# Kernel optimization log

Hardware: AMD Instinct MI355X
Metric: run time of the kernel (lower is better)

Reference implementation:

```python
import jax, jax.numpy as jnp
import numpy as np


def lrelu(x):
    return jnp.where(x > 0, x, 0.1 * x)


def setup_inputs() -> dict:
    key = jax.random.key(0)
    ks = jax.random.split(key, 16)
    L, B, E = 160, 16, 512
    C, H, DM, DO = 256, 512, 128, 512  # conv channels, enc_hid, d_mlp, dec_hid

    def rn(k, shape, scale=0.05):
        return jax.random.normal(k, shape, dtype=jnp.float32) * scale

    return {
        "x": rn(ks[0], (L, B, E), 1.0),
        "h": rn(ks[1], (B, H), 1.0),
        "conv_w": rn(ks[2], (C, E, 3)),
        "conv_b": rn(ks[3], (C,)),
        "bn_g": jnp.ones((C,), jnp.float32),
        "bn_b": jnp.zeros((C,), jnp.float32),
        "W1": rn(ks[4], (DM, 2 * (C + 2) + H)),
        "b1": rn(ks[5], (DM,)),
        "W2": rn(ks[6], (DM, DM)), "b2": rn(ks[7], (DM,)),
        "W3": rn(ks[8], (DM, DM)), "b3": rn(ks[9], (DM,)),
        "W4": rn(ks[10], (DM, DM)), "b4": rn(ks[11], (DM,)),
        "W5": rn(ks[12], (DM, DM)), "b5": rn(ks[13], (DM,)),
        "W6": rn(ks[14], (DO, DM)), "b6": rn(ks[15], (DO,)),
    }


def reference(x, h, conv_w, conv_b, bn_g, bn_b,
              W1, b1, W2, b2, W3, b3, W4, b4, W5, b5, W6, b6):
    L, B, E = x.shape
    # --- ConvLayer: Conv1d(k=3, pad=1) -> LeakyReLU(0.1) -> BatchNorm1d (training stats)
    xc = jnp.transpose(x, (1, 2, 0))  # (B, E, L)
    y = jax.lax.conv_general_dilated(xc, conv_w, (1,), [(1, 1)],
                                     dimension_numbers=("NCH", "OIH", "NCH"))
    y = lrelu(y + conv_b[None, :, None])
    mu = y.mean(axis=(0, 2), keepdims=True)
    var = y.var(axis=(0, 2), keepdims=True)  # biased variance (torch training BN)
    y = (y - mu) * jax.lax.rsqrt(var + 1e-5)
    y = y * bn_g[None, :, None] + bn_b[None, :, None]
    y = jnp.transpose(y, (0, 2, 1))  # (B, L, C)

    # --- coordinate features: [(i/sqrt(L)-2)/2, (i % sqrt(L) - 2)/2]
    sL = np.sqrt(L)
    i = jnp.arange(L, dtype=jnp.float32)
    coords = jnp.stack([(i / sL - 2.0) / 2.0, (jnp.mod(i, sL) - 2.0) / 2.0], axis=-1)  # (L, 2)
    xf = jnp.concatenate([y, jnp.broadcast_to(coords[None], (B, L, 2))], axis=-1)  # (B, L, C+2)
    Cp = xf.shape[-1]

    # --- g_mlp first Linear decomposed over [x_i | x_j | h] feature blocks:
    # x_i[b,a,c] = xf[b,c] (varies with dim2); x_j[b,a,c] = cat(xf[b,a], h[b]) (varies with dim1)
    W1i = W1[:, :Cp]            # acts on x_i
    W1jx = W1[:, Cp:2 * Cp]     # acts on x part of x_j
    W1jh = W1[:, 2 * Cp:]       # acts on h part of x_j
    u = jnp.einsum('blc,dc->bld', xf, W1i)                     # (B, L, DM), index = dim2
    v = jnp.einsum('blc,dc->bld', xf, W1jx) + (h @ W1jh.T)[:, None, :]  # (B, L, DM), index = dim1
    z = lrelu(v[:, :, None, :] + u[:, None, :, :] + b1)        # (B, L, L, DM)
    z = lrelu(z @ W2.T + b2)
    z = lrelu(z @ W3.T + b3)
    z = lrelu(z @ W4.T + b4)
    s = z.sum(axis=(1, 2))  # sum over all L*L pairs -> (B, DM)

    # --- f_mlp
    s = lrelu(s @ W5.T + b5)
    return lrelu(s @ W6.T + b6)  # (B, dec_hid)
```

## Files before the change

### kernel.cpp

```cpp
#include <hip/hip_runtime.h>
#include <cstdint>

typedef unsigned short u16;
typedef uint32_t u32;

typedef __bf16 bf16x8 __attribute__((ext_vector_type(8)));
typedef float  f32x2  __attribute__((ext_vector_type(2)));
typedef float  f32x4  __attribute__((ext_vector_type(4)));
typedef float  f32x16 __attribute__((ext_vector_type(16)));
typedef u16    u16x4  __attribute__((ext_vector_type(4)));
typedef u16    u16x8  __attribute__((ext_vector_type(8)));

__device__ __forceinline__ u16 f2bf(float f) {
    u32 x = __float_as_uint(f);
    return (u16)((x + 0x7FFFu + ((x >> 16) & 1u)) >> 16);
}
__device__ __forceinline__ float lrelu(float x) { return fmaxf(x, 0.1f * x); }

__device__ __forceinline__ u32 pack_rn(float lo, float hi) {
    u32 a = __float_as_uint(lo) + 0x8000u;
    u32 b = __float_as_uint(hi) + 0x8000u;
    return __builtin_amdgcn_perm(b, a, 0x07060302u);
}

__global__ __launch_bounds__(256) void k_prep(
    const float* __restrict__ x, const float* __restrict__ conv_w,
    const float* __restrict__ W2, const float* __restrict__ W3, const float* __restrict__ W4,
    const float* __restrict__ b2, const float* __restrict__ b3, const float* __restrict__ b4,
    const float* __restrict__ h, const float* __restrict__ W1,
    u16* __restrict__ xb, u16* __restrict__ wcb_f, u16* __restrict__ wfrag,
    float* __restrict__ W1T4, float* __restrict__ hW, float* __restrict__ zero0)
{
    int blk = blockIdx.x, tid = threadIdx.x;
    if (blk < 1280) {
        int o = (blk * 256 + tid) * 4;
        int e = o & 511;
        int bl = o >> 9;
        int b = bl / 160, l = bl % 160;
        f32x4 v = *(const f32x4*)(x + ((size_t)(l * 16 + b)) * 512 + e);
        u16x4 ov;
        ov[0] = f2bf(v[0]); ov[1] = f2bf(v[1]); ov[2] = f2bf(v[2]); ov[3] = f2bf(v[3]);
        *(u16x4*)&xb[o] = ov;
    } else if (blk < 1472) {
        int g = (blk - 1280) * 256 + tid;
        int lane = g & 63;
        int ks = (g >> 6) % 48;
        int cb = g / 3072;
        int c = cb * 16 + (lane & 15);
        int quad = lane >> 4;
        int k0 = ks * 32 + quad * 8;
        int tap = k0 >> 9, e0 = k0 & 511;
        u16x8 ov;
        #pragma unroll
        for (int j = 0; j < 8; j++)
            ov[j] = f2bf(conv_w[((size_t)c * 512 + e0 + j) * 3 + tap]);
        *(u16x8*)&wcb_f[(size_t)g * 8] = ov;
    } else if (blk < 1526) {
        int o = ((blk - 1472) * 256 + tid) * 4;
        int layer = o / 18432, rem = o % 18432;
        int ks9 = rem >> 11;
        int rem2 = rem & 2047;
        int hh = rem2 >> 10;
        int rem3 = rem2 & 1023;
        int n = rem3 >> 3, j0 = rem3 & 7;
        const float* W = (layer == 0) ? W2 : (layer == 1) ? W3 : W4;
        const float* bi = (layer == 0) ? b2 : (layer == 1) ? b3 : b4;
        u16x4 ov;
        if (ks9 < 8) {
            f32x4 v = *(const f32x4*)(W + (size_t)n * 128 + 16 * ks9 + 8 * hh + j0);
            ov[0] = f2bf(v[0]); ov[1] = f2bf(v[1]); ov[2] = f2bf(v[2]); ov[3] = f2bf(v[3]);
        } else {
            ov[0] = (hh == 0 && j0 == 0) ? f2bf(bi[n]) : (u16)0;
            ov[1] = 0; ov[2] = 0; ov[3] = 0;
        }
        *(u16x4*)&wfrag[o] = ov;
    } else if (blk < 1591) {
        int cq = blk - 1526;
        int t = tid;
        const float* src = (t < 128)
            ? (W1 + (size_t)t * 1028 + cq * 4)
            : (W1 + (size_t)(t - 128) * 1028 + 258 + cq * 4);
        f32x2 v0 = *(const f32x2*)src;
        f32x2 v1 = *(const f32x2*)(src + 2);
        f32x4 v;
        v[0] = v0[0]; v[1] = v0[1];
        v[2] = (cq == 64) ? 0.f : v1[0];
        v[3] = (cq == 64) ? 0.f : v1[1];
        *(f32x4*)&W1T4[((size_t)cq * 256 + t) * 4] = v;
    } else if (blk < 1719) {
        int gid = (blk - 1591) * 256 + tid;
        int outp = gid >> 4, q = gid & 15;
        int b = outp >> 7, d = outp & 127;
        const float* hr = h + (size_t)b * 512;
        const float* wr = W1 + (size_t)d * 1028 + 516;
        float acc = 0.f;
        #pragma unroll
        for (int c = 0; c < 8; c++) {
            int k = c * 64 + q * 4;
            f32x4 hv = *(const f32x4*)(hr + k);
            f32x4 wv = *(const f32x4*)(wr + k);
            acc += hv[0]*wv[0] + hv[1]*wv[1] + hv[2]*wv[2] + hv[3]*wv[3];
        }
        acc += __shfl_xor(acc, 1); acc += __shfl_xor(acc, 2);
        acc += __shfl_xor(acc, 4); acc += __shfl_xor(acc, 8);
        if (q == 0) hW[outp] = acc;
    } else {
        int idx = (blk - 1719) * 256 + tid;
        if (idx < 640) {
            f32x4 z = {0.f, 0.f, 0.f, 0.f};
            *(f32x4*)&zero0[idx * 4] = z;
        }
    }
}

__global__ __launch_bounds__(256, 4) void k_conv(
    const u16* __restrict__ xb, const u16* __restrict__ wcb_f,
    const float* __restrict__ conv_b,
    float* __restrict__ ws_y, float* __restrict__ stats)
{
    __shared__ u16 xs[18 * 520];
    int tid = threadIdx.x, wg = blockIdx.x;
    int rowtile = wg >> 2, cg = wg & 3;
    int b = rowtile / 10, l0 = (rowtile % 10) * 16;

    for (int t = tid; t < 18 * 64; t += 256) {
        int s = t >> 6, ch = t & 63;
        int lg = l0 + s - 1;
        u16x8 v = {};
        if (lg >= 0 && lg < 160)
            v = *(const u16x8*)(xb + ((size_t)(b * 160 + lg)) * 512 + ch * 8);
        *(u16x8*)&xs[s * 520 + ch * 8] = v;
    }
    __syncthreads();

    int lane = tid & 63, w = tid >> 6;
    int row16 = lane & 15, quad = lane >> 4;
    int cb = cg * 4 + w;
    int c_n = cb * 16 + row16;
    const u16* wb = wcb_f + (size_t)cb * 24576;

    f32x4 acc0 = {0,0,0,0};
    for (int ks4 = 0; ks4 < 48; ks4 += 4) {
        bf16x8 wf[4];
        #pragma unroll
        for (int q = 0; q < 4; q++)
            wf[q] = *(const bf16x8*)(wb + (size_t)((ks4 + q) * 64 + lane) * 8);
        #pragma unroll
        for (int q = 0; q < 4; q++) {
            int k = (ks4 + q) * 32 + quad * 8;
            int tap = k >> 9, e = k & 511;
            bf16x8 a0 = *(const bf16x8*)&xs[(row16 + tap) * 520 + e];
            acc0 = __builtin_amdgcn_mfma_f32_16x16x32_bf16(a0, wf[q], acc0, 0, 0, 0);
        }
    }

    float bias = conv_b[c_n];
    float sum = 0.f, sq = 0.f;
    #pragma unroll
    for (int r = 0; r < 4; r++) {
        float v = lrelu(acc0[r] + bias);
        int lr = l0 + quad * 4 + r;
        ws_y[((size_t)(b * 160 + lr)) * 256 + c_n] = v;
        sum += v; sq += v * v;
    }
    sum += __shfl_xor(sum, 16); sum += __shfl_xor(sum, 32);
    sq  += __shfl_xor(sq, 16);  sq  += __shfl_xor(sq, 32);
    if (quad == 0) {
        atomicAdd(&stats[c_n], sum);
        atomicAdd(&stats[256 + c_n], sq);
    }
}

__global__ __launch_bounds__(256) void k_uv(
    const float* __restrict__ ws_y, const float* __restrict__ stats,
    const float* __restrict__ bn_g, const float* __restrict__ bn_b,
    const float* __restrict__ W1T4, const float* __restrict__ b1,
    const float* __restrict__ hW,
    float* __restrict__ uu, float* __restrict__ vv)
{
    __shared__ float a_s[256], c_s[256];
    __shared__ float xfs[4 * 260];
    int tid = threadIdx.x;
    int row0 = blockIdx.x * 4;
    int b = row0 / 160, l0 = row0 % 160;
    {
        int c = tid;
        float mu  = stats[c] * (1.0f / 2560.0f);
        float var = stats[256 + c] * (1.0f / 2560.0f) - mu * mu;
        float rs  = rsqrtf(var + 1e-5f) * bn_g[c];
        a_s[c] = rs;
        c_s[c] = bn_b[c] - mu * rs;
    }
    __syncthreads();
    float sLf = sqrtf(160.0f);
    for (int idx = tid; idx < 4 * 260; idx += 256) {
        int r = idx / 260, c = idx - r * 260;
        int l = l0 + r;
        float v = 0.f;
        if (c < 256) {
            v = ws_y[((size_t)(b * 160 + l)) * 256 + c] * a_s[c] + c_s[c];
        } else if (c == 256) {
            v = ((float)l / sLf - 2.0f) * 0.5f;
        } else if (c == 257) {
            float fi = (float)l;
            float m = fi - floorf(fi / sLf) * sLf;
            v = (m - 2.0f) * 0.5f;
        }
        xfs[r * 260 + c] = v;
    }
    __syncthreads();

    float acc[4] = {0,0,0,0};
    #pragma unroll 4
    for (int cq = 0; cq < 65; cq++) {
        f32x4 w4 = *(const f32x4*)&W1T4[((size_t)cq * 256 + tid) * 4];
        #pragma unroll
        for (int r = 0; r < 4; r++) {
            f32x4 xv = *(const f32x4*)&xfs[r * 260 + cq * 4];
            acc[r] += w4[0]*xv[0] + w4[1]*xv[1] + w4[2]*xv[2] + w4[3]*xv[3];
        }
    }

    bool isv = tid >= 128;
    int d = tid & 127;
    float vadd = isv ? (hW[b * 128 + d] + b1[d]) : 0.f;
    float* dst = isv ? vv : uu;
    #pragma unroll
    for (int r = 0; r < 4; r++)
        dst[((size_t)(b * 160 + l0 + r)) * 128 + d] = acc[r] + vadd;
}

__global__ __launch_bounds__(256, 4) void k_mlp(
    const float* __restrict__ vv, const float* __restrict__ uu,
    const u16* __restrict__ wfrag,
    float* __restrict__ s_glob)
{
    __shared__ __align__(16) u16 Wlds[18432];
    __shared__ float spart[128];
    int tid = threadIdx.x;
    int wave = tid >> 6, lane = tid & 63;
    int h = lane >> 5, lo = lane & 31;
    int b = blockIdx.x / 200, sub = blockIdx.x % 200;
    int tileb = sub * 4 + wave;

    if (tid < 128) spart[tid] = 0.f;

    u32 selv = h ? 0x07060302u : 0x05040100u;
    uint4 biasfrag;
    biasfrag.x = (h == 0) ? 0x00003F80u : 0u;
    biasfrag.y = 0u; biasfrag.z = 0u; biasfrag.w = 0u;

    uint4 B[8];
    f32x16 acc[4];
    float ssum[4];

    int i  = (tileb / 10) * 2  + (lo >> 4);
    int jj = (tileb % 10) * 16 + (lo & 15);
    const float* vr = vv + ((size_t)(b * 160 + i))  * 128 + 8 * h;
    const float* ur = uu + ((size_t)(b * 160 + jj)) * 128 + 8 * h;

    for (int layer = 0; layer < 3; layer++) {
        __syncthreads();
        {
            const uint4* src = (const uint4*)(wfrag + layer * 18432);
            #pragma unroll
            for (int it = 0; it < 9; it++) {
                int idx = it * 256 + tid;
                *(uint4*)&Wlds[idx * 8] = src[idx];
            }
        }
        __syncthreads();

        if (layer == 0) {
            #pragma unroll
            for (int ks = 0; ks < 8; ks++) {
                f32x4 v0 = *(const f32x4*)(vr + 16 * ks);
                f32x4 v1 = *(const f32x4*)(vr + 16 * ks + 4);
                f32x4 u0 = *(const f32x4*)(ur + 16 * ks);
                f32x4 u1 = *(const f32x4*)(ur + 16 * ks + 4);
                uint4 d;
                d.x = pack_rn(lrelu(v0[0]+u0[0]), lrelu(v0[1]+u0[1]));
                d.y = pack_rn(lrelu(v0[2]+u0[2]), lrelu(v0[3]+u0[3]));
                d.z = pack_rn(lrelu(v1[0]+u1[0]), lrelu(v1[1]+u1[1]));
                d.w = pack_rn(lrelu(v1[2]+u1[2]), lrelu(v1[3]+u1[3]));
                B[ks] = d;
            }
        }

        #pragma unroll
        for (int nt = 0; nt < 4; nt++)
            #pragma unroll
            for (int r = 0; r < 16; r++) acc[nt][r] = 0.f;

        #pragma unroll
        for (int ks = 0; ks < 9; ks++) {
            uint4 zu = (ks < 8) ? B[ks] : biasfrag;
            bf16x8 zf = *(bf16x8*)&zu;
            #pragma unroll
            for (int nt = 0; nt < 4; nt++) {
                bf16x8 wf = *(const bf16x8*)&Wlds[(size_t)(ks * 256 + h * 128 + nt * 32 + lo) * 8];
                if (layer < 2)
                    acc[nt] = __builtin_amdgcn_mfma_f32_32x32x16_bf16(wf, zf, acc[nt], 0, 0, 0);
                else
                    acc[nt] = __builtin_amdgcn_mfma_f32_32x32x16_bf16(zf, wf, acc[nt], 0, 0, 0);
            }
        }

        if (layer < 2) {
            #pragma unroll
            for (int nt = 0; nt < 4; nt++) {
                u32 own[4][2], oth[4][2];
                #pragma unroll
                for (int c = 0; c < 4; c++)
                    #pragma unroll
                    for (int p = 0; p < 2; p++)
                        own[c][p] = pack_rn(lrelu(acc[nt][c + 8*p]),
                                            lrelu(acc[nt][c + 4 + 8*p]));
                #pragma unroll
                for (int c = 0; c < 4; c++)
                    #pragma unroll
                    for (int p = 0; p < 2; p++)
                        oth[c][p] = (u32)__shfl_xor((int)own[c][p], 32);
                #pragma unroll
                for (int p = 0; p < 2; p++) {
                    u32 dA0 = __builtin_amdgcn_perm(own[1][p], own[0][p], selv);
                    u32 dB0 = __builtin_amdgcn_perm(oth[1][p], oth[0][p], selv);
                    u32 dA1 = __builtin_amdgcn_perm(own[3][p], own[2][p], selv);
                    u32 dB1 = __builtin_amdgcn_perm(oth[3][p], oth[2][p], selv);
                    uint4 d;
                    d.x = h ? dB0 : dA0;
                    d.y = h ? dB1 : dA1;
                    d.z = h ? dA0 : dB0;
                    d.w = h ? dA1 : dB1;
                    B[2 * nt + p] = d;
                }
            }
        } else {
            #pragma unroll
            for (int nt = 0; nt < 4; nt++) {
                float t = 0.f;
                #pragma unroll
                for (int r = 0; r < 16; r++)
                    t += lrelu(acc[nt][r]);
                ssum[nt] = t;
            }
        }
    }

    #pragma unroll
    for (int nt = 0; nt < 4; nt++) {
        float v = ssum[nt] + __shfl_xor(ssum[nt], 32);
        if (h == 0) atomicAdd(&spart[nt * 32 + lo], v);
    }
    __syncthreads();
    if (tid < 128) atomicAdd(&s_glob[b * 128 + tid], spart[tid]);
}

__global__ __launch_bounds__(256) void k_final(
    const float* __restrict__ s_glob,
    const float* __restrict__ W5, const float* __restrict__ b5,
    const float* __restrict__ W6, const float* __restrict__ b6,
    float* __restrict__ out)
{
    __shared__ float sh[128], t5[128];
    int b = blockIdx.x, tid = threadIdx.x;
    if (tid < 128) sh[tid] = s_glob[b * 128 + tid];
    __syncthreads();
    if (tid < 128) {
        const float* wr = W5 + (size_t)tid * 128;
        float acc = b5[tid];
        #pragma unroll
        for (int k = 0; k < 128; k += 4) {
            f32x4 wv = *(const f32x4*)(wr + k);
            f32x4 sv = *(const f32x4*)&sh[k];
            acc += wv[0]*sv[0] + wv[1]*sv[1] + wv[2]*sv[2] + wv[3]*sv[3];
        }
        t5[tid] = lrelu(acc);
    }
    __syncthreads();
    #pragma unroll
    for (int q = 0; q < 2; q++) {
        int o = q * 256 + tid;
        const float* wr = W6 + (size_t)o * 128;
        float acc = b6[o];
        #pragma unroll
        for (int k = 0; k < 128; k += 4) {
            f32x4 wv = *(const f32x4*)(wr + k);
            f32x4 tv = *(const f32x4*)&t5[k];
            acc += wv[0]*tv[0] + wv[1]*tv[1] + wv[2]*tv[2] + wv[3]*tv[3];
        }
        out[b * 512 + o] = lrelu(acc);
    }
}

extern "C" void kernel_launch(void* const* d_in, const int* in_sizes, int n_in,
                              void* d_out, int out_size, void* d_ws, size_t ws_size,
                              hipStream_t stream)
{
    const float* x      = (const float*)d_in[0];
    const float* h      = (const float*)d_in[1];
    const float* conv_w = (const float*)d_in[2];
    const float* conv_b = (const float*)d_in[3];
    const float* bn_g   = (const float*)d_in[4];
    const float* bn_b   = (const float*)d_in[5];
    const float* W1     = (const float*)d_in[6];
    const float* b1     = (const float*)d_in[7];
    const float* W2     = (const float*)d_in[8];
    const float* b2     = (const float*)d_in[9];
    const float* W3     = (const float*)d_in[10];
    const float* b3     = (const float*)d_in[11];
    const float* W4     = (const float*)d_in[12];
    const float* b4     = (const float*)d_in[13];
    const float* W5     = (const float*)d_in[14];
    const float* b5     = (const float*)d_in[15];
    const float* W6     = (const float*)d_in[16];
    const float* b6     = (const float*)d_in[17];

    char* ws = (char*)d_ws;
    float* s_glob = (float*)(ws + 0);
    float* stats  = (float*)(ws + 8192);
    float* hW     = (float*)(ws + 10240);
    float* ws_y   = (float*)(ws + 18432);
    float* vv     = (float*)(ws + 2639872);
    float* uu     = (float*)(ws + 3950592);
    u16*   xb     = (u16*)  (ws + 5261312);
    u16*   wcb_f  = (u16*)  (ws + 7882752);
    u16*   wfrag  = (u16*)  (ws + 8669184);
    float* W1T4   = (float*)(ws + 8779776);

    k_prep <<<1722, 256, 0, stream>>>(x, conv_w, W2, W3, W4, b2, b3, b4, h, W1,
                                      xb, wcb_f, wfrag, W1T4, hW, s_glob);
    k_conv <<<640, 256, 0, stream>>>(xb, wcb_f, conv_b, ws_y, stats);
    k_uv   <<<640, 256, 0, stream>>>(ws_y, stats, bn_g, bn_b, W1T4, b1, hW, uu, vv);
    k_mlp  <<<3200, 256, 0, stream>>>(vv, uu, wfrag, s_glob);
    k_final<<<16, 256, 0, stream>>>(s_glob, W5, b5, W6, b6, (float*)d_out);
}
```

Baseline: 217.3 us.

## Process two pair tiles per wave in MLP kernel to reuse weight fragments

After: 229.1 us. 5.4% more time.

```diff
diff --git a/kernel.cpp b/kernel.cpp
--- a/kernel.cpp
+++ b/kernel.cpp
@@ -230,7 +230,7 @@
         dst[((size_t)(b * 160 + l0 + r)) * 128 + d] = acc[r] + vadd;
 }
 
-__global__ __launch_bounds__(256, 4) void k_mlp(
+__global__ __launch_bounds__(256, 2) void k_mlp(
     const float* __restrict__ vv, const float* __restrict__ uu,
     const u16* __restrict__ wfrag,
     float* __restrict__ s_glob)
@@ -240,8 +240,8 @@
     int tid = threadIdx.x;
     int wave = tid >> 6, lane = tid & 63;
     int h = lane >> 5, lo = lane & 31;
-    int b = blockIdx.x / 200, sub = blockIdx.x % 200;
-    int tileb = sub * 4 + wave;
+    int b = blockIdx.x / 100, sub = blockIdx.x % 100;
+    int t0 = sub * 8 + wave * 2;
 
     if (tid < 128) spart[tid] = 0.f;
 
@@ -250,14 +250,20 @@
     biasfrag.x = (h == 0) ? 0x00003F80u : 0u;
     biasfrag.y = 0u; biasfrag.z = 0u; biasfrag.w = 0u;
 
-    uint4 B[8];
-    f32x16 acc[4];
-    float ssum[4];
-
-    int i  = (tileb / 10) * 2  + (lo >> 4);
-    int jj = (tileb % 10) * 16 + (lo & 15);
-    const float* vr = vv + ((size_t)(b * 160 + i))  * 128 + 8 * h;
-    const float* ur = uu + ((size_t)(b * 160 + jj)) * 128 + 8 * h;
+    f32x16 Z;
+    #pragma unroll
+    for (int r = 0; r < 16; r++) Z[r] = 0.f;
+
+    uint4 B0[8], B1[8], N0[8], N1[8];
+    float ssum[2][4];
+
+    int ta = t0, tb = t0 + 1;
+    int ia = (ta / 10) * 2 + (lo >> 4), ja = (ta % 10) * 16 + (lo & 15);
+    int ib = (tb / 10) * 2 + (lo >> 4), jb = (tb % 10) * 16 + (lo & 15);
+    const float* vra = vv + ((size_t)(b * 160 + ia)) * 128 + 8 * h;
+    const float* ura = uu + ((size_t)(b * 160 + ja)) * 128 + 8 * h;
+    const float* vrb = vv + ((size_t)(b * 160 + ib)) * 128 + 8 * h;
+    const float* urb = uu + ((size_t)(b * 160 + jb)) * 128 + 8 * h;
 
     for (int layer = 0; layer < 3; layer++) {
         __syncthreads();
@@ -274,82 +280,100 @@
         if (layer == 0) {
             #pragma unroll
             for (int ks = 0; ks < 8; ks++) {
-                f32x4 v0 = *(const f32x4*)(vr + 16 * ks);
-                f32x4 v1 = *(const f32x4*)(vr + 16 * ks + 4);
-                f32x4 u0 = *(const f32x4*)(ur + 16 * ks);
-                f32x4 u1 = *(const f32x4*)(ur + 16 * ks + 4);
+                f32x4 v0 = *(const f32x4*)(vra + 16 * ks);
+                f32x4 v1 = *(const f32x4*)(vra + 16 * ks + 4);
+                f32x4 u0 = *(const f32x4*)(ura + 16 * ks);
+                f32x4 u1 = *(const f32x4*)(ura + 16 * ks + 4);
                 uint4 d;
                 d.x = pack_rn(lrelu(v0[0]+u0[0]), lrelu(v0[1]+u0[1]));
                 d.y = pack_rn(lrelu(v0[2]+u0[2]), lrelu(v0[3]+u0[3]));
                 d.z = pack_rn(lrelu(v1[0]+u1[0]), lrelu(v1[1]+u1[1]));
                 d.w = pack_rn(lrelu(v1[2]+u1[2]), lrelu(v1[3]+u1[3]));
-                B[ks] = d;
+                B0[ks] = d;
+                f32x4 w0 = *(const f32x4*)(vrb + 16 * ks);
+                f32x4 w1 = *(const f32x4*)(vrb + 16 * ks + 4);
+                f32x4 y0 = *(const f32x4*)(urb + 16 * ks);
+                f32x4 y1 = *(const f32x4*)(urb + 16 * ks + 4);
+                uint4 e;
+                e.x = pack_rn(lrelu(w0[0]+y0[0]), lrelu(w0[1]+y0[1]));
+                e.y = pack_rn(lrelu(w0[2]+y0[2]), lrelu(w0[3]+y0[3]));
+                e.z = pack_rn(lrelu(w1[0]+y1[0]), lrelu(w1[1]+y1[1]));
+                e.w = pack_rn(lrelu(w1[2]+y1[2]), lrelu(w1[3]+y1[3]));
+                B1[ks] = e;
             }
         }
 
         #pragma unroll
-        for (int nt = 0; nt < 4; nt++)
+        for (int nt = 0; nt < 4; nt++) {
+            f32x16 a0, a1;
             #pragma unroll
-            for (int r = 0; r < 16; r++) acc[nt][r] = 0.f;
-
-        #pragma unroll
-        for (int ks = 0; ks < 9; ks++) {
-            uint4 zu = (ks < 8) ? B[ks] : biasfrag;
-            bf16x8 zf = *(bf16x8*)&zu;
-            #pragma unroll
-            for (int nt = 0; nt < 4; nt++) {
+            for (int ks = 0; ks < 9; ks++) {
                 bf16x8 wf = *(const bf16x8*)&Wlds[(size_t)(ks * 256 + h * 128 + nt * 32 + lo) * 8];
-                if (layer < 2)
-                    acc[nt] = __builtin_amdgcn_mfma_f32_32x32x16_bf16(wf, zf, acc[nt], 0, 0, 0);
-                else
-                    acc[nt] = __builtin_amdgcn_mfma_f32_32x32x16_bf16(zf, wf, acc[nt], 0, 0, 0);
+                uint4 z0u = (ks < 8) ? B0[ks] : biasfrag;
+                uint4 z1u = (ks < 8) ? B1[ks] : biasfrag;
+                bf16x8 zf0 = *(bf16x8*)&z0u;
+                bf16x8 zf1 = *(bf16x8*)&z1u;
+                if (layer < 2) {
+                    a0 = __builtin_amdgcn_mfma_f32_32x32x16_bf16(wf, zf0, ks ? a0 : Z, 0, 0, 0);
+                    a1 = __builtin_amdgcn_mfma_f32_32x32x16_bf16(wf, zf1, ks ? a1 : Z, 0, 0, 0);
+                } else {
+                    a0 = __builtin_amdgcn_mfma_f32_32x32x16_bf16(zf0, wf, ks ? a0 : Z, 0, 0, 0);
+                    a1 = __builtin_amdgcn_mfma_f32_32x32x16_bf16(zf1, wf, ks ? a1 : Z, 0, 0, 0);
+                }
+            }
+
+            if (layer < 2) {
+                #pragma unroll
+                for (int s = 0; s < 2; s++) {
+                    const f32x16& a = s ? a1 : a0;
+                    u32 own[4][2], oth[4][2];
+                    #pragma unroll
+                    for (int c = 0; c < 4; c++)
+                        #pragma unroll
+                        for (int p = 0; p < 2; p++)
+                            own[c][p] = pack_rn(lrelu(a[c + 8*p]),
+                                                lrelu(a[c + 4 + 8*p]));
+                    #pragma unroll
+                    for (int c = 0; c < 4; c++)
+                        #pragma unroll
+                        for (int p = 0; p < 2; p++)
+                            oth[c][p] = (u32)__shfl_xor((int)own[c][p], 32);
+                    #pragma unroll
+                    for (int p = 0; p < 2; p++) {
+                        u32 dA0 = __builtin_amdgcn_perm(own[1][p], own[0][p], selv);
+                        u32 dB0 = __builtin_amdgcn_perm(oth[1][p], oth[0][p], selv);
+                        u32 dA1 = __builtin_amdgcn_perm(own[3][p], own[2][p], selv);
+                        u32 dB1 = __builtin_amdgcn_perm(oth[3][p], oth[2][p], selv);
+                        uint4 d;
+                        d.x = h ? dB0 : dA0;
+                        d.y = h ? dB1 : dA1;
+                        d.z = h ? dA0 : dB0;
+                        d.w = h ? dA1 : dB1;
+                        if (s) N1[2 * nt + p] = d; else N0[2 * nt + p] = d;
+                    }
+                }
+            } else {
+                float s0 = 0.f, s1 = 0.f;
+                #pragma unroll
+                for (int r = 0; r < 16; r++) {
+                    s0 += lrelu(a0[r]);
+                    s1 += lrelu(a1[r]);
+                }
+                ssum[0][nt] = s0;
+                ssum[1][nt] = s1;
             }
         }
 
         if (layer < 2) {
             #pragma unroll
-            for (int nt = 0; nt < 4; nt++) {
-                u32 own[4][2], oth[4][2];
-                #pragma unroll
-                for (int c = 0; c < 4; c++)
-                    #pragma unroll
-                    for (int p = 0; p < 2; p++)
-                        own[c][p] = pack_rn(lrelu(acc[nt][c + 8*p]),
-                                            lrelu(acc[nt][c + 4 + 8*p]));
-                #pragma unroll
-                for (int c = 0; c < 4; c++)
-                    #pragma unroll
-                    for (int p = 0; p < 2; p++)
-                        oth[c][p] = (u32)__shfl_xor((int)own[c][p], 32);
-                #pragma unroll
-                for (int p = 0; p < 2; p++) {
-                    u32 dA0 = __builtin_amdgcn_perm(own[1][p], own[0][p], selv);
-                    u32 dB0 = __builtin_amdgcn_perm(oth[1][p], oth[0][p], selv);
-                    u32 dA1 = __builtin_amdgcn_perm(own[3][p], own[2][p], selv);
-                    u32 dB1 = __builtin_amdgcn_perm(oth[3][p], oth[2][p], selv);
-                    uint4 d;
-                    d.x = h ? dB0 : dA0;
-                    d.y = h ? dB1 : dA1;
-                    d.z = h ? dA0 : dB0;
-                    d.w = h ? dA1 : dB1;
-                    B[2 * nt + p] = d;
-                }
-            }
-        } else {
-            #pragma unroll
-            for (int nt = 0; nt < 4; nt++) {
-                float t = 0.f;
-                #pragma unroll
-                for (int r = 0; r < 16; r++)
-                    t += lrelu(acc[nt][r]);
-                ssum[nt] = t;
-            }
+            for (int ks = 0; ks < 8; ks++) { B0[ks] = N0[ks]; B1[ks] = N1[ks]; }
         }
     }
 
     #pragma unroll
     for (int nt = 0; nt < 4; nt++) {
-        float v = ssum[nt] + __shfl_xor(ssum[nt], 32);
+        float v = ssum[0][nt] + ssum[1][nt];
+        v += __shfl_xor(v, 32);
         if (h == 0) atomicAdd(&spart[nt * 32 + lo], v);
     }
     __syncthreads();
@@ -432,6 +456,6 @@
                                       xb, wcb_f, wfrag, W1T4, hW, s_glob);
     k_conv <<<640, 256, 0, stream>>>(xb, wcb_f, conv_b, ws_y, stats);
     k_uv   <<<640, 256, 0, stream>>>(ws_y, stats, bn_g, bn_b, W1T4, b1, hW, uu, vv);
-    k_mlp  <<<3200, 256, 0, stream>>>(vv, uu, wfrag, s_glob);
+    k_mlp  <<<1600, 256, 0, stream>>>(vv, uu, wfrag, s_glob);
     k_final<<<16, 256, 0, stream>>>(s_glob, W5, b5, W6, b6, (float*)d_out);
 }
```

## Use bf16 MFMA for u/v projection and restructure MLP accumulators per n-tile

Applied to the files above, without the earlier changes.

After: 193.2 us. -11.1%, faster.

```diff
diff --git a/kernel.cpp b/kernel.cpp
--- a/kernel.cpp
+++ b/kernel.cpp
@@ -29,7 +29,7 @@
     const float* __restrict__ b2, const float* __restrict__ b3, const float* __restrict__ b4,
     const float* __restrict__ h, const float* __restrict__ W1,
     u16* __restrict__ xb, u16* __restrict__ wcb_f, u16* __restrict__ wfrag,
-    float* __restrict__ W1T4, float* __restrict__ hW, float* __restrict__ zero0)
+    u16* __restrict__ w1frag, float* __restrict__ hW, float* __restrict__ zero0)
 {
     int blk = blockIdx.x, tid = threadIdx.x;
     if (blk < 1280) {
@@ -74,21 +74,26 @@
             ov[1] = 0; ov[2] = 0; ov[3] = 0;
         }
         *(u16x4*)&wfrag[o] = ov;
-    } else if (blk < 1591) {
-        int cq = blk - 1526;
-        int t = tid;
-        const float* src = (t < 128)
-            ? (W1 + (size_t)t * 1028 + cq * 4)
-            : (W1 + (size_t)(t - 128) * 1028 + 258 + cq * 4);
-        f32x2 v0 = *(const f32x2*)src;
-        f32x2 v1 = *(const f32x2*)(src + 2);
-        f32x4 v;
-        v[0] = v0[0]; v[1] = v0[1];
-        v[2] = (cq == 64) ? 0.f : v1[0];
-        v[3] = (cq == 64) ? 0.f : v1[1];
-        *(f32x4*)&W1T4[((size_t)cq * 256 + t) * 4] = v;
-    } else if (blk < 1719) {
-        int gid = (blk - 1591) * 256 + tid;
+    } else if (blk < 1598) {
+        int o = ((blk - 1526) * 256 + tid) * 4;
+        int nt = o / 4608;
+        int rem = o % 4608;
+        int ks = rem >> 9;
+        int rem2 = rem & 511;
+        int lane = rem2 >> 3, j0 = rem2 & 7;
+        int n = nt * 16 + (lane & 15);
+        int k0 = ks * 32 + (lane >> 4) * 8 + j0;
+        const float* wr = (n < 128) ? (W1 + (size_t)n * 1028)
+                                    : (W1 + (size_t)(n - 128) * 1028 + 258);
+        u16x4 ov;
+        #pragma unroll
+        for (int q = 0; q < 4; q++) {
+            int k = k0 + q;
+            ov[q] = (k < 258) ? f2bf(wr[k]) : (u16)0;
+        }
+        *(u16x4*)&w1frag[o] = ov;
+    } else if (blk < 1726) {
+        int gid = (blk - 1598) * 256 + tid;
         int outp = gid >> 4, q = gid & 15;
         int b = outp >> 7, d = outp & 127;
         const float* hr = h + (size_t)b * 512;
@@ -105,7 +110,7 @@
         acc += __shfl_xor(acc, 4); acc += __shfl_xor(acc, 8);
         if (q == 0) hW[outp] = acc;
     } else {
-        int idx = (blk - 1719) * 256 + tid;
+        int idx = (blk - 1726) * 256 + tid;
         if (idx < 640) {
             f32x4 z = {0.f, 0.f, 0.f, 0.f};
             *(f32x4*)&zero0[idx * 4] = z;
@@ -174,14 +179,14 @@
 __global__ __launch_bounds__(256) void k_uv(
     const float* __restrict__ ws_y, const float* __restrict__ stats,
     const float* __restrict__ bn_g, const float* __restrict__ bn_b,
-    const float* __restrict__ W1T4, const float* __restrict__ b1,
+    const u16* __restrict__ w1frag, const float* __restrict__ b1,
     const float* __restrict__ hW,
     float* __restrict__ uu, float* __restrict__ vv)
 {
     __shared__ float a_s[256], c_s[256];
-    __shared__ float xfs[4 * 260];
+    __shared__ __align__(16) u16 xfs[16 * 296];
     int tid = threadIdx.x;
-    int row0 = blockIdx.x * 4;
+    int row0 = blockIdx.x * 16;
     int b = row0 / 160, l0 = row0 % 160;
     {
         int c = tid;
@@ -193,8 +198,8 @@
     }
     __syncthreads();
     float sLf = sqrtf(160.0f);
-    for (int idx = tid; idx < 4 * 260; idx += 256) {
-        int r = idx / 260, c = idx - r * 260;
+    for (int idx = tid; idx < 16 * 288; idx += 256) {
+        int r = idx / 288, c = idx - r * 288;
         int l = l0 + r;
         float v = 0.f;
         if (c < 256) {
@@ -206,28 +211,44 @@
             float m = fi - floorf(fi / sLf) * sLf;
             v = (m - 2.0f) * 0.5f;
         }
-        xfs[r * 260 + c] = v;
-    }
-    __syncthreads();
-
-    float acc[4] = {0,0,0,0};
-    #pragma unroll 4
-    for (int cq = 0; cq < 65; cq++) {
-        f32x4 w4 = *(const f32x4*)&W1T4[((size_t)cq * 256 + tid) * 4];
+        xfs[r * 296 + c] = f2bf(v);
+    }
+    __syncthreads();
+
+    int lane = tid & 63, w = tid >> 6;
+    int row16 = lane & 15, quad = lane >> 4;
+
+    bf16x8 af[9];
+    #pragma unroll
+    for (int ks = 0; ks < 9; ks++)
+        af[ks] = *(const bf16x8*)&xfs[row16 * 296 + ks * 32 + quad * 8];
+
+    f32x4 acc[4];
+    #pragma unroll
+    for (int nt = 0; nt < 4; nt++) {
+        f32x4 a = {0.f, 0.f, 0.f, 0.f};
+        #pragma unroll
+        for (int ks = 0; ks < 9; ks++) {
+            bf16x8 bf = *(const bf16x8*)(w1frag +
+                (size_t)(((w * 4 + nt) * 9 + ks) * 64 + lane) * 8);
+            a = __builtin_amdgcn_mfma_f32_16x16x32_bf16(af[ks], bf, a, 0, 0, 0);
+        }
+        acc[nt] = a;
+    }
+
+    #pragma unroll
+    for (int nt = 0; nt < 4; nt++) {
+        int n = (w * 4 + nt) * 16 + row16;
+        bool isv = n >= 128;
+        int d = n & 127;
+        float add = isv ? (hW[b * 128 + d] + b1[d]) : 0.f;
+        float* dst = isv ? vv : uu;
         #pragma unroll
         for (int r = 0; r < 4; r++) {
-            f32x4 xv = *(const f32x4*)&xfs[r * 260 + cq * 4];
-            acc[r] += w4[0]*xv[0] + w4[1]*xv[1] + w4[2]*xv[2] + w4[3]*xv[3];
-        }
-    }
-
-    bool isv = tid >= 128;
-    int d = tid & 127;
-    float vadd = isv ? (hW[b * 128 + d] + b1[d]) : 0.f;
-    float* dst = isv ? vv : uu;
-    #pragma unroll
-    for (int r = 0; r < 4; r++)
-        dst[((size_t)(b * 160 + l0 + r)) * 128 + d] = acc[r] + vadd;
+            int l = l0 + quad * 4 + r;
+            dst[((size_t)(b * 160 + l)) * 128 + d] = acc[nt][r] + add;
+        }
+    }
 }
 
 __global__ __launch_bounds__(256, 4) void k_mlp(
@@ -250,8 +271,11 @@
     biasfrag.x = (h == 0) ? 0x00003F80u : 0u;
     biasfrag.y = 0u; biasfrag.z = 0u; biasfrag.w = 0u;
 
-    uint4 B[8];
-    f32x16 acc[4];
+    f32x16 Z;
+    #pragma unroll
+    for (int r = 0; r < 16; r++) Z[r] = 0.f;
+
+    uint4 B[8], Bn[8];
     float ssum[4];
 
     int i  = (tileb / 10) * 2  + (lo >> 4);
@@ -288,34 +312,27 @@
         }
 
         #pragma unroll
-        for (int nt = 0; nt < 4; nt++)
+        for (int nt = 0; nt < 4; nt++) {
+            f32x16 a;
             #pragma unroll
-            for (int r = 0; r < 16; r++) acc[nt][r] = 0.f;
-
-        #pragma unroll
-        for (int ks = 0; ks < 9; ks++) {
-            uint4 zu = (ks < 8) ? B[ks] : biasfrag;
-            bf16x8 zf = *(bf16x8*)&zu;
-            #pragma unroll
-            for (int nt = 0; nt < 4; nt++) {
+            for (int ks = 0; ks < 9; ks++) {
                 bf16x8 wf = *(const bf16x8*)&Wlds[(size_t)(ks * 256 + h * 128 + nt * 32 + lo) * 8];
+                uint4 zu = (ks < 8) ? B[ks] : biasfrag;
+                bf16x8 zf = *(bf16x8*)&zu;
                 if (layer < 2)
-                    acc[nt] = __builtin_amdgcn_mfma_f32_32x32x16_bf16(wf, zf, acc[nt], 0, 0, 0);
+                    a = __builtin_amdgcn_mfma_f32_32x32x16_bf16(wf, zf, ks ? a : Z, 0, 0, 0);
                 else
-                    acc[nt] = __builtin_amdgcn_mfma_f32_32x32x16_bf16(zf, wf, acc[nt], 0, 0, 0);
+                    a = __builtin_amdgcn_mfma_f32_32x32x16_bf16(zf, wf, ks ? a : Z, 0, 0, 0);
             }
-        }
-
-        if (layer < 2) {
-            #pragma unroll
-            for (int nt = 0; nt < 4; nt++) {
+
+            if (layer < 2) {
                 u32 own[4][2], oth[4][2];
                 #pragma unroll
                 for (int c = 0; c < 4; c++)
                     #pragma unroll
                     for (int p = 0; p < 2; p++)
-                        own[c][p] = pack_rn(lrelu(acc[nt][c + 8*p]),
-                                            lrelu(acc[nt][c + 4 + 8*p]));
+                        own[c][p] = pack_rn(lrelu(a[c + 8*p]),
+                                            lrelu(a[c + 4 + 8*p]));
                 #pragma unroll
                 for (int c = 0; c < 4; c++)
                     #pragma unroll
@@ -332,18 +349,20 @@
                     d.y = h ? dB1 : dA1;
                     d.z = h ? dA0 : dB0;
                     d.w = h ? dA1 : dB1;
-                    B[2 * nt + p] = d;
+                    Bn[2 * nt + p] = d;
                 }
-            }
-        } else {
-            #pragma unroll
-            for (int nt = 0; nt < 4; nt++) {
+            } else {
                 float t = 0.f;
                 #pragma unroll
                 for (int r = 0; r < 16; r++)
-                    t += lrelu(acc[nt][r]);
+                    t += lrelu(a[r]);
                 ssum[nt] = t;
             }
+        }
+
+        if (layer < 2) {
+            #pragma unroll
+            for (int ks = 0; ks < 8; ks++) B[ks] = Bn[ks];
         }
     }
 
@@ -426,12 +445,12 @@
     u16*   xb     = (u16*)  (ws + 5261312);
     u16*   wcb_f  = (u16*)  (ws + 7882752);
     u16*   wfrag  = (u16*)  (ws + 8669184);
-    float* W1T4   = (float*)(ws + 8779776);
-
-    k_prep <<<1722, 256, 0, stream>>>(x, conv_w, W2, W3, W4, b2, b3, b4, h, W1,
-                                      xb, wcb_f, wfrag, W1T4, hW, s_glob);
+    u16*   w1frag = (u16*)  (ws + 8779776);
+
+    k_prep <<<1729, 256, 0, stream>>>(x, conv_w, W2, W3, W4, b2, b3, b4, h, W1,
+                                      xb, wcb_f, wfrag, w1frag, hW, s_glob);
     k_conv <<<640, 256, 0, stream>>>(xb, wcb_f, conv_b, ws_y, stats);
-    k_uv   <<<640, 256, 0, stream>>>(ws_y, stats, bn_g, bn_b, W1T4, b1, hW, uu, vv);
+    k_uv   <<<160, 256, 0, stream>>>(ws_y, stats, bn_g, bn_b, w1frag, b1, hW, uu, vv);
     k_mlp  <<<3200, 256, 0, stream>>>(vv, uu, wfrag, s_glob);
     k_final<<<16, 256, 0, stream>>>(s_glob, W5, b5, W6, b6, (float*)d_out);
 }
```
